# Optimization experiments

Measured on AMD Instinct MI355X. Metric: run time of the kernel, lower is better.

Reference implementation:

```python
import jax, jax.numpy as jnp
import numpy as np

B, N, K, E = 2, 131072, 20, 256  # batch, points, n_slot, feat/embed dim
GN_GROUPS = 4
IOU_THR = 0.5
SCORE_THR = 0.04
TEMP = 0.05


def setup_inputs() -> dict:
    key = jax.random.key(0)
    ks = jax.random.split(key, 6)
    wscale = 1.0 / np.sqrt(E)
    return {
        "features": jax.random.normal(ks[0], (B, N, E), jnp.float32),
        "slots": jax.random.normal(ks[1], (B, K, E), jnp.float32),
        "w1": jax.random.normal(ks[2], (E, E), jnp.float32) * wscale,
        "b1": jax.random.normal(ks[3], (E,), jnp.float32) * 0.01,
        "gn_g": jnp.ones((E,), jnp.float32),
        "gn_b": jnp.zeros((E,), jnp.float32),
        "w2": jax.random.normal(ks[4], (E, E), jnp.float32) * wscale,
        "b2": jax.random.normal(ks[5], (E,), jnp.float32) * 0.01,
    }


def _l2norm(x, axis):
    n = jnp.linalg.norm(x, axis=axis, keepdims=True)
    return x / jnp.maximum(n, 1e-12)  # F.normalize semantics


def _nms_filter(mask):
    # mask: [N, K] soft instance probabilities (rows sum to 1)
    scores = mask.mean(axis=0)                       # [K]
    valid = scores >= SCORE_THR
    order = jnp.argsort(-scores)                     # descending score
    sm = mask[:, order]                              # [N, K] sorted columns
    bm = (sm > 0.5).astype(mask.dtype).T             # [K, N] binary masks
    areas = bm.sum(axis=1)                           # [K]
    inter = bm @ bm.T                                # [K, K] pairwise intersections
    union = areas[:, None] + areas[None, :] - inter
    iou = inter / (union + 1e-8)
    idx = jnp.arange(K)
    sup0 = ~valid[order]                             # invalid slots pre-suppressed

    def body(i, sup):
        keep_i = ~sup[i]
        return sup | (keep_i & (iou[i] > IOU_THR) & (idx > i))

    sup = jax.lax.fori_loop(0, K, body, sup0)
    kept = ~sup                                      # [K]
    # kept columns are packed (in score order) into the left of the output;
    # dropped columns are routed to a dump column K which is sliced away.
    pos = jnp.cumsum(kept) - 1
    cols = jnp.where(kept, pos, K)
    out = jnp.zeros((mask.shape[0], K + 1), mask.dtype).at[:, cols].set(sm)
    out = out[:, :K]
    # per-point renormalization over kept masks (zeros stay zero if none kept)
    return out / (out.sum(axis=1, keepdims=True) + 1e-8)


def reference(features, slots, w1, b1, gn_g, gn_b, w2, b2):
    # object_mlp: Conv1d(1x1) -> GroupNorm(4) -> ReLU -> Conv1d(1x1)
    x = jnp.einsum('bke,oe->bok', slots, w1) + b1[None, :, None]   # [B, E, K]
    xg = x.reshape(B, GN_GROUPS, E // GN_GROUPS, K)
    mu = xg.mean(axis=(2, 3), keepdims=True)
    var = xg.var(axis=(2, 3), keepdims=True)
    xg = (xg - mu) * jax.lax.rsqrt(var + 1e-5)
    x = xg.reshape(B, E, K) * gn_g[None, :, None] + gn_b[None, :, None]
    x = jax.nn.relu(x)
    slot = jnp.einsum('bek,fe->bfk', x, w2) + b2[None, :, None]    # [B, F=E, K]

    fn = _l2norm(features, axis=-1)                                # [B, N, E]
    sn = _l2norm(slot, axis=1)                                     # [B, E, K]
    logits = jnp.einsum('bnd,bdk->bnk', fn, sn) / TEMP
    mask = jax.nn.softmax(logits, axis=-1)                         # [B, N, K]

    out = jax.vmap(_nms_filter)(mask)                              # [B, N, K]
    return out.transpose(0, 2, 1)                                  # [B, K, N]
```

## Files before the change

kernel.cpp:

```cpp
#include <hip/hip_runtime.h>

#define B_ 2
#define N_ 131072
#define K_ 20
#define E_ 256
#define TEMP_ 0.05f
#define SCORE_THR_ 0.04f

#define WS_SCORE 0
#define WS_XN    1024
#define WS_SN    16384
#define WS_MASK  32768

__device__ inline float wave_sum(float v) {
    #pragma unroll
    for (int off = 32; off; off >>= 1) v += __shfl_xor(v, off, 64);
    return v;
}

__global__ __launch_bounds__(256) void kA1(const float* __restrict__ slots,
                                           const float* __restrict__ w1,
                                           const float* __restrict__ b1,
                                           const float* __restrict__ gn_g,
                                           const float* __restrict__ gn_b,
                                           float* __restrict__ ws) {
    __shared__ __align__(16) float slds[20 * 260];
    __shared__ float red[2];
    const int t = threadIdx.x;
    const int b = blockIdx.x >> 2, g = blockIdx.x & 3;
    if (t < 5) ws[WS_SCORE + blockIdx.x * 5 + t] = 0.f;
    if (t < 2) red[t] = 0.f;
    const float* sb = slots + (size_t)b * K_ * E_;
    #pragma unroll
    for (int i = 0; i < 20; ++i) slds[i * 260 + t] = sb[i * 256 + t];
    __syncthreads();

    const int c = t >> 2, q = t & 3;
    const int o = g * 64 + c;
    const float* w1r = w1 + (size_t)o * E_;
    float acc[5] = {0.f, 0.f, 0.f, 0.f, 0.f};
    for (int e4 = 0; e4 < 64; ++e4) {
        const float4 w4 = *(const float4*)(w1r + e4 * 4);
        #pragma unroll
        for (int kk = 0; kk < 5; ++kk) {
            const float4 s4 = *(const float4*)&slds[(q * 5 + kk) * 260 + e4 * 4];
            acc[kk] += w4.x * s4.x + w4.y * s4.y + w4.z * s4.z + w4.w * s4.w;
        }
    }
    const float bias = b1[o];
    float s1 = 0.f, s2 = 0.f;
    #pragma unroll
    for (int kk = 0; kk < 5; ++kk) {
        acc[kk] += bias;
        s1 += acc[kk];
        s2 += acc[kk] * acc[kk];
    }
    s1 = wave_sum(s1);
    s2 = wave_sum(s2);
    if ((t & 63) == 0) { atomicAdd(&red[0], s1); atomicAdd(&red[1], s2); }
    __syncthreads();
    const float mean = red[0] * (1.f / 1280.f);
    const float var  = red[1] * (1.f / 1280.f) - mean * mean;
    const float rstd = rsqrtf(var + 1e-5f);
    const float gg = gn_g[o], gb = gn_b[o];
    float* xn = ws + WS_XN + (size_t)b * K_ * E_;
    #pragma unroll
    for (int kk = 0; kk < 5; ++kk) {
        float v = (acc[kk] - mean) * rstd * gg + gb;
        v = v > 0.f ? v : 0.f;
        xn[(q * 5 + kk) * 256 + o] = v;
    }
}

__global__ __launch_bounds__(256) void kA2(const float* __restrict__ w2,
                                           const float* __restrict__ b2,
                                           float* __restrict__ ws) {
    __shared__ __align__(16) float xv[256];
    __shared__ float wred[4];
    const int t = threadIdx.x;
    const int b = blockIdx.x / 20, k = blockIdx.x % 20;
    const float* xn = ws + WS_XN + (size_t)(b * 20 + k) * 256;
    xv[t] = xn[t];
    __syncthreads();
    const float* w2r = w2 + (size_t)t * 256;
    float acc = 0.f;
    for (int e4 = 0; e4 < 64; ++e4) {
        const float4 w4 = *(const float4*)(w2r + e4 * 4);
        const float4 x4 = *(const float4*)&xv[e4 * 4];
        acc += w4.x * x4.x + w4.y * x4.y + w4.z * x4.z + w4.w * x4.w;
    }
    acc += b2[t];
    float sq = wave_sum(acc * acc);
    if ((t & 63) == 0) wred[t >> 6] = sq;
    __syncthreads();
    const float nsq = wred[0] + wred[1] + wred[2] + wred[3];
    const float inv = 1.f / fmaxf(sqrtf(nsq), 1e-12f);
    ws[WS_SN + (size_t)(b * 20 + k) * 256 + t] = acc * inv;
}

__global__ __launch_bounds__(256) void kB(const float* __restrict__ feat,
                                          float* __restrict__ ws) {
    __shared__ __align__(16) float snl[5120];
    __shared__ float wsum[4][20];
    const int t = threadIdx.x;
    const int b = blockIdx.x >> 8;
    const int n0 = (blockIdx.x & 255) * 512;
    const float* sng = ws + WS_SN + (size_t)b * 5120;
    #pragma unroll
    for (int i = 0; i < 20; ++i) snl[i * 256 + t] = sng[i * 256 + t];
    __syncthreads();

    const float* p0 = feat + ((size_t)b * N_ + n0 + t) * E_;
    const float* p1 = p0 + 256 * E_;
    float acc0[20], acc1[20];
    #pragma unroll
    for (int k = 0; k < 20; ++k) { acc0[k] = 0.f; acc1[k] = 0.f; }
    float nr0 = 0.f, nr1 = 0.f;

    float4 a0 = *(const float4*)(p0);
    float4 a1 = *(const float4*)(p1);
    float4 b0 = *(const float4*)(p0 + 4);
    float4 b1v = *(const float4*)(p1 + 4);
    for (int j = 0; j < 64; j += 2) {
        const int jn = (j + 2 < 64) ? (j + 2) : 62;
        const float4 na0 = *(const float4*)(p0 + jn * 4);
        const float4 na1 = *(const float4*)(p1 + jn * 4);
        const float4 nb0 = *(const float4*)(p0 + jn * 4 + 4);
        const float4 nb1 = *(const float4*)(p1 + jn * 4 + 4);

        nr0 += a0.x * a0.x + a0.y * a0.y + a0.z * a0.z + a0.w * a0.w;
        nr1 += a1.x * a1.x + a1.y * a1.y + a1.z * a1.z + a1.w * a1.w;
        #pragma unroll
        for (int k = 0; k < 20; ++k) {
            const float4 s4 = *(const float4*)&snl[k * 256 + j * 4];
            acc0[k] += a0.x * s4.x + a0.y * s4.y + a0.z * s4.z + a0.w * s4.w;
            acc1[k] += a1.x * s4.x + a1.y * s4.y + a1.z * s4.z + a1.w * s4.w;
        }
        nr0 += b0.x * b0.x + b0.y * b0.y + b0.z * b0.z + b0.w * b0.w;
        nr1 += b1v.x * b1v.x + b1v.y * b1v.y + b1v.z * b1v.z + b1v.w * b1v.w;
        #pragma unroll
        for (int k = 0; k < 20; ++k) {
            const float4 s4 = *(const float4*)&snl[k * 256 + j * 4 + 4];
            acc0[k] += b0.x * s4.x + b0.y * s4.y + b0.z * s4.z + b0.w * s4.w;
            acc1[k] += b1v.x * s4.x + b1v.y * s4.y + b1v.z * s4.z + b1v.w * s4.w;
        }
        a0 = na0; a1 = na1; b0 = nb0; b1v = nb1;
    }

    const float sc0 = rsqrtf(fmaxf(nr0, 1e-24f)) * (1.f / TEMP_);
    const float sc1 = rsqrtf(fmaxf(nr1, 1e-24f)) * (1.f / TEMP_);
    float m0 = -1e30f, m1 = -1e30f;
    #pragma unroll
    for (int k = 0; k < 20; ++k) {
        acc0[k] *= sc0; acc1[k] *= sc1;
        m0 = fmaxf(m0, acc0[k]); m1 = fmaxf(m1, acc1[k]);
    }
    float su0 = 0.f, su1 = 0.f;
    #pragma unroll
    for (int k = 0; k < 20; ++k) {
        acc0[k] = __expf(acc0[k] - m0); su0 += acc0[k];
        acc1[k] = __expf(acc1[k] - m1); su1 += acc1[k];
    }
    const float r0 = 1.f / su0, r1 = 1.f / su1;
    float* mg = ws + WS_MASK + (size_t)b * 20 * N_ + n0 + t;
    #pragma unroll
    for (int k = 0; k < 20; ++k) {
        const float v0 = acc0[k] * r0;
        const float v1 = acc1[k] * r1;
        mg[(size_t)k * N_] = v0;
        mg[(size_t)k * N_ + 256] = v1;
        acc0[k] = v0 + v1;
    }
    #pragma unroll
    for (int k = 0; k < 20; ++k) acc0[k] = wave_sum(acc0[k]);
    const int wid = t >> 6, lid = t & 63;
    if (lid == 0) {
        #pragma unroll
        for (int k = 0; k < 20; ++k) wsum[wid][k] = acc0[k];
    }
    __syncthreads();
    if (t < 20) {
        const float s = wsum[0][t] + wsum[1][t] + wsum[2][t] + wsum[3][t];
        atomicAdd(&ws[WS_SCORE + b * 20 + t], s);
    }
}

__global__ __launch_bounds__(256) void kD(const float* __restrict__ ws,
                                          float* __restrict__ out) {
    __shared__ float sc[20];
    __shared__ int rnk[20];
    __shared__ int src[20];
    __shared__ int nk_s;
    const int t = threadIdx.x;
    const int b = blockIdx.x >> 9;
    const int n = (blockIdx.x & 511) * 256 + t;
    if (t < 20) sc[t] = ws[WS_SCORE + b * 20 + t] * (1.f / (float)N_);
    if (t == 0) nk_s = 0;
    __syncthreads();
    if (t < 20) {
        const float mys = sc[t];
        int rank = 0;
        for (int j = 0; j < 20; ++j) {
            const float o = sc[j];
            rank += (o > mys) || (o == mys && j < t);
        }
        rnk[t] = rank;
    }
    __syncthreads();
    if (t < 20 && sc[t] >= SCORE_THR_) {
        int pos = 0;
        for (int j = 0; j < 20; ++j)
            pos += (sc[j] >= SCORE_THR_) && (rnk[j] < rnk[t]);
        src[pos] = t;
        atomicAdd(&nk_s, 1);
    }
    __syncthreads();
    const int nk = nk_s;
    const float* mg = ws + WS_MASK + (size_t)b * 20 * N_;
    float mv[20];
    float den = 1e-8f;
    #pragma unroll
    for (int p = 0; p < 20; ++p) {
        float v = 0.f;
        if (p < nk) v = mg[(size_t)src[p] * N_ + n];
        mv[p] = v;
        den += v;
    }
    const float r = 1.f / den;
    float* og = out + (size_t)b * 20 * N_ + n;
    #pragma unroll
    for (int p = 0; p < 20; ++p) og[(size_t)p * N_] = (p < nk) ? mv[p] * r : 0.f;
}

extern "C" void kernel_launch(void* const* d_in, const int* in_sizes, int n_in,
                              void* d_out, int out_size, void* d_ws, size_t ws_size,
                              hipStream_t stream) {
    const float* feat  = (const float*)d_in[0];
    const float* slots = (const float*)d_in[1];
    const float* w1    = (const float*)d_in[2];
    const float* b1    = (const float*)d_in[3];
    const float* gng   = (const float*)d_in[4];
    const float* gnb   = (const float*)d_in[5];
    const float* w2    = (const float*)d_in[6];
    const float* b2    = (const float*)d_in[7];
    float* ws  = (float*)d_ws;
    float* out = (float*)d_out;

    kA1<<<8,    256, 0, stream>>>(slots, w1, b1, gng, gnb, ws);
    kA2<<<40,   256, 0, stream>>>(w2, b2, ws);
    kB <<<512,  256, 0, stream>>>(feat, ws);
    kD <<<1024, 256, 0, stream>>>(ws, out);
}
```

Measured before the change: 442.3 us.

## Stage feature tiles through LDS with coalesced loads and deterministic score reduction

The similarity kernel now loads 32-point feature tiles cooperatively with coalesced float4 reads into padded LDS. Eight threads then split each point's 256-dim dot products and combine them with shuffle reductions. Mask writes are transposed through LDS so stores along N are contiguous. Global atomics on slot scores are replaced by per-block partial sums plus a small reduction kernel. This removes the strided per-thread row reads of the old layout, at the cost of extra barriers, shuffle traffic and one more launch.

```diff
diff --git a/kernel.cpp b/kernel.cpp
--- a/kernel.cpp
+++ b/kernel.cpp
@@ -11,6 +11,7 @@
 #define WS_XN    1024
 #define WS_SN    16384
 #define WS_MASK  32768
+#define WS_SPART 6291456
 
 __device__ inline float wave_sum(float v) {
     #pragma unroll
@@ -28,7 +29,6 @@
     __shared__ float red[2];
     const int t = threadIdx.x;
     const int b = blockIdx.x >> 2, g = blockIdx.x & 3;
-    if (t < 5) ws[WS_SCORE + blockIdx.x * 5 + t] = 0.f;
     if (t < 2) red[t] = 0.f;
     const float* sb = slots + (size_t)b * K_ * E_;
     #pragma unroll
@@ -98,91 +98,117 @@
     ws[WS_SN + (size_t)(b * 20 + k) * 256 + t] = acc * inv;
 }
 
-__global__ __launch_bounds__(256) void kB(const float* __restrict__ feat,
-                                          float* __restrict__ ws) {
-    __shared__ __align__(16) float snl[5120];
+__global__ __launch_bounds__(256, 2) void kB(const float* __restrict__ feat,
+                                             float* __restrict__ ws) {
+    __shared__ __align__(16) float snl[20 * 260];
+    __shared__ __align__(16) float fl[32 * 260];
+    __shared__ float pl[640];
     __shared__ float wsum[4][20];
     const int t = threadIdx.x;
-    const int b = blockIdx.x >> 8;
-    const int n0 = (blockIdx.x & 255) * 512;
+    const int b = blockIdx.x >> 9;
+    const int n0 = (blockIdx.x & 511) << 8;
     const float* sng = ws + WS_SN + (size_t)b * 5120;
     #pragma unroll
-    for (int i = 0; i < 20; ++i) snl[i * 256 + t] = sng[i * 256 + t];
-    __syncthreads();
-
-    const float* p0 = feat + ((size_t)b * N_ + n0 + t) * E_;
-    const float* p1 = p0 + 256 * E_;
-    float acc0[20], acc1[20];
-    #pragma unroll
-    for (int k = 0; k < 20; ++k) { acc0[k] = 0.f; acc1[k] = 0.f; }
-    float nr0 = 0.f, nr1 = 0.f;
-
-    float4 a0 = *(const float4*)(p0);
-    float4 a1 = *(const float4*)(p1);
-    float4 b0 = *(const float4*)(p0 + 4);
-    float4 b1v = *(const float4*)(p1 + 4);
-    for (int j = 0; j < 64; j += 2) {
-        const int jn = (j + 2 < 64) ? (j + 2) : 62;
-        const float4 na0 = *(const float4*)(p0 + jn * 4);
-        const float4 na1 = *(const float4*)(p1 + jn * 4);
-        const float4 nb0 = *(const float4*)(p0 + jn * 4 + 4);
-        const float4 nb1 = *(const float4*)(p1 + jn * 4 + 4);
-
-        nr0 += a0.x * a0.x + a0.y * a0.y + a0.z * a0.z + a0.w * a0.w;
-        nr1 += a1.x * a1.x + a1.y * a1.y + a1.z * a1.z + a1.w * a1.w;
-        #pragma unroll
-        for (int k = 0; k < 20; ++k) {
-            const float4 s4 = *(const float4*)&snl[k * 256 + j * 4];
-            acc0[k] += a0.x * s4.x + a0.y * s4.y + a0.z * s4.z + a0.w * s4.w;
-            acc1[k] += a1.x * s4.x + a1.y * s4.y + a1.z * s4.z + a1.w * s4.w;
-        }
-        nr0 += b0.x * b0.x + b0.y * b0.y + b0.z * b0.z + b0.w * b0.w;
-        nr1 += b1v.x * b1v.x + b1v.y * b1v.y + b1v.z * b1v.z + b1v.w * b1v.w;
-        #pragma unroll
-        for (int k = 0; k < 20; ++k) {
-            const float4 s4 = *(const float4*)&snl[k * 256 + j * 4 + 4];
-            acc0[k] += b0.x * s4.x + b0.y * s4.y + b0.z * s4.z + b0.w * s4.w;
-            acc1[k] += b1v.x * s4.x + b1v.y * s4.y + b1v.z * s4.z + b1v.w * s4.w;
-        }
-        a0 = na0; a1 = na1; b0 = nb0; b1v = nb1;
-    }
-
-    const float sc0 = rsqrtf(fmaxf(nr0, 1e-24f)) * (1.f / TEMP_);
-    const float sc1 = rsqrtf(fmaxf(nr1, 1e-24f)) * (1.f / TEMP_);
-    float m0 = -1e30f, m1 = -1e30f;
-    #pragma unroll
-    for (int k = 0; k < 20; ++k) {
-        acc0[k] *= sc0; acc1[k] *= sc1;
-        m0 = fmaxf(m0, acc0[k]); m1 = fmaxf(m1, acc1[k]);
-    }
-    float su0 = 0.f, su1 = 0.f;
-    #pragma unroll
-    for (int k = 0; k < 20; ++k) {
-        acc0[k] = __expf(acc0[k] - m0); su0 += acc0[k];
-        acc1[k] = __expf(acc1[k] - m1); su1 += acc1[k];
-    }
-    const float r0 = 1.f / su0, r1 = 1.f / su1;
-    float* mg = ws + WS_MASK + (size_t)b * 20 * N_ + n0 + t;
-    #pragma unroll
-    for (int k = 0; k < 20; ++k) {
-        const float v0 = acc0[k] * r0;
-        const float v1 = acc1[k] * r1;
-        mg[(size_t)k * N_] = v0;
-        mg[(size_t)k * N_ + 256] = v1;
-        acc0[k] = v0 + v1;
-    }
-    #pragma unroll
-    for (int k = 0; k < 20; ++k) acc0[k] = wave_sum(acc0[k]);
-    const int wid = t >> 6, lid = t & 63;
-    if (lid == 0) {
-        #pragma unroll
-        for (int k = 0; k < 20; ++k) wsum[wid][k] = acc0[k];
+    for (int i = 0; i < 20; ++i) snl[i * 260 + t] = sng[i * 256 + t];
+    const int p = t >> 3, s = t & 7;
+    const int lane = t & 63, w = t >> 6;
+    float sreg0 = 0.f, sreg1 = 0.f, sreg2 = 0.f;
+    const float4* gbase = (const float4*)(feat + ((size_t)b * N_ + n0) * E_);
+    float* mgbase = ws + WS_MASK + (size_t)b * 20 * N_ + n0;
+    __syncthreads();
+
+    for (int c = 0; c < 8; ++c) {
+        const float4* g4 = gbase + (size_t)c * 2048;
+        #pragma unroll
+        for (int i = 0; i < 8; ++i) {
+            const int idx = t + (i << 8);
+            const float4 v = g4[idx];
+            const int pp = idx >> 6, cc = idx & 63;
+            *(float4*)&fl[pp * 260 + (cc << 2)] = v;
+        }
+        __syncthreads();
+        float acc[20];
+        float nr = 0.f;
+        #pragma unroll
+        for (int k = 0; k < 20; ++k) acc[k] = 0.f;
+        const float* frow = &fl[p * 260];
+        #pragma unroll
+        for (int j = 0; j < 8; ++j) {
+            const int col = (s << 2) + (j << 5);
+            const float4 f4 = *(const float4*)&frow[col];
+            nr += f4.x * f4.x + f4.y * f4.y + f4.z * f4.z + f4.w * f4.w;
+            #pragma unroll
+            for (int k = 0; k < 20; ++k) {
+                const float4 s4 = *(const float4*)&snl[k * 260 + col];
+                acc[k] += f4.x * s4.x + f4.y * s4.y + f4.z * s4.z + f4.w * s4.w;
+            }
+        }
+        #pragma unroll
+        for (int off = 1; off < 8; off <<= 1) {
+            nr += __shfl_xor(nr, off, 64);
+            #pragma unroll
+            for (int k = 0; k < 20; ++k) acc[k] += __shfl_xor(acc[k], off, 64);
+        }
+        const float scl = rsqrtf(fmaxf(nr, 1e-24f)) * (1.f / TEMP_);
+        float m = -1e30f;
+        #pragma unroll
+        for (int k = 0; k < 20; ++k) { acc[k] *= scl; m = fmaxf(m, acc[k]); }
+        float su = 0.f;
+        #pragma unroll
+        for (int k = 0; k < 20; ++k) { acc[k] = __expf(acc[k] - m); su += acc[k]; }
+        const float r = 1.f / su;
+        float v0 = 0.f, v1 = 0.f, v2 = 0.f;
+        #pragma unroll
+        for (int k = 0; k < 8; ++k) {
+            if (s == k) {
+                v0 = acc[k] * r;
+                v1 = acc[k + 8] * r;
+                v2 = (k < 4) ? acc[k + 16] * r : 0.f;
+            }
+        }
+        pl[(s << 5) + p] = v0;
+        pl[((s + 8) << 5) + p] = v1;
+        if (s < 4) pl[((s + 16) << 5) + p] = v2;
+        sreg0 += v0; sreg1 += v1; sreg2 += v2;
+        __syncthreads();
+        #pragma unroll
+        for (int i = 0; i < 3; ++i) {
+            const int idx = t + (i << 8);
+            if (idx < 640) {
+                const int k = idx >> 5, pp = idx & 31;
+                mgbase[(size_t)k * N_ + (c << 5) + pp] = pl[idx];
+            }
+        }
+        __syncthreads();
+    }
+    #pragma unroll
+    for (int off = 8; off < 64; off <<= 1) {
+        sreg0 += __shfl_xor(sreg0, off, 64);
+        sreg1 += __shfl_xor(sreg1, off, 64);
+        sreg2 += __shfl_xor(sreg2, off, 64);
+    }
+    if (lane < 8) {
+        wsum[w][lane] = sreg0;
+        wsum[w][lane + 8] = sreg1;
+        if (lane < 4) wsum[w][lane + 16] = sreg2;
     }
     __syncthreads();
     if (t < 20) {
-        const float s = wsum[0][t] + wsum[1][t] + wsum[2][t] + wsum[3][t];
-        atomicAdd(&ws[WS_SCORE + b * 20 + t], s);
-    }
+        const float sum = wsum[0][t] + wsum[1][t] + wsum[2][t] + wsum[3][t];
+        ws[WS_SPART + (size_t)blockIdx.x * 20 + t] = sum;
+    }
+}
+
+__global__ __launch_bounds__(64) void kC(float* __restrict__ ws) {
+    const int l = threadIdx.x;
+    const int b = blockIdx.x / 20, k = blockIdx.x % 20;
+    const float* sp = ws + WS_SPART;
+    float sum = 0.f;
+    #pragma unroll
+    for (int i = 0; i < 8; ++i)
+        sum += sp[(size_t)(b * 512 + l + i * 64) * 20 + k];
+    sum = wave_sum(sum);
+    if (l == 0) ws[WS_SCORE + blockIdx.x] = sum * (1.f / (float)N_);
 }
 
 __global__ __launch_bounds__(256) void kD(const float* __restrict__ ws,
@@ -194,7 +220,7 @@
     const int t = threadIdx.x;
     const int b = blockIdx.x >> 9;
     const int n = (blockIdx.x & 511) * 256 + t;
-    if (t < 20) sc[t] = ws[WS_SCORE + b * 20 + t] * (1.f / (float)N_);
+    if (t < 20) sc[t] = ws[WS_SCORE + b * 20 + t];
     if (t == 0) nk_s = 0;
     __syncthreads();
     if (t < 20) {
@@ -248,6 +274,7 @@
 
     kA1<<<8,    256, 0, stream>>>(slots, w1, b1, gng, gnb, ws);
     kA2<<<40,   256, 0, stream>>>(w2, b2, ws);
-    kB <<<512,  256, 0, stream>>>(feat, ws);
+    kB <<<1024, 256, 0, stream>>>(feat, ws);
+    kC <<<40,   64,  0, stream>>>(ws);
     kD <<<1024, 256, 0, stream>>>(ws, out);
 }
```

Result: faster. 431.9 us (-2.4%).
